# Performance work log

Hardware: AMD Instinct MI355X
Metric: run time of the kernel (lower is better)

## Reference

```python
import jax, jax.numpy as jnp
import numpy as np

N_NODES = 100000
N_GRAPHS = 64


def gcn_conv(x, src, dst, W, b, num_nodes):
    """PyG GCNConv: add self-loops, symmetric deg normalization, aggregate at dst."""
    h = x @ W  # [N, out]
    ones_e = jnp.ones(src.shape[0], dtype=x.dtype)
    # degree includes self-loop (+1)
    deg = jax.ops.segment_sum(ones_e, dst, num_segments=num_nodes) + 1.0
    dinv = jnp.where(deg > 0, 1.0 / jnp.sqrt(deg), 0.0)  # deg>=1 always here
    norm = dinv[src] * dinv[dst]  # [E]
    msg = h[src] * norm[:, None]  # gather + scale
    agg = jax.ops.segment_sum(msg, dst, num_segments=num_nodes)
    # self-loop contribution: norm_ii = dinv[i]^2
    agg = agg + h * (dinv * dinv)[:, None]
    return agg + b


def global_mean_pool(x, batch, num_graphs):
    sums = jax.ops.segment_sum(x, batch, num_segments=num_graphs)
    counts = jax.ops.segment_sum(jnp.ones(x.shape[0], dtype=x.dtype), batch,
                                 num_segments=num_graphs)
    return sums / jnp.maximum(counts, 1.0)[:, None]


def setup_inputs() -> dict:
    key = jax.random.key(0)
    ks = jax.random.split(key, 8)
    H = 128
    x = jax.random.normal(ks[0], (N_NODES, 4), dtype=jnp.float32)
    edge_index = jax.random.randint(ks[1], (2, 1600000), 0, N_NODES, dtype=jnp.int64 if jax.config.read('jax_enable_x64') else jnp.int32)
    batch = jnp.sort(jax.random.randint(ks[2], (N_NODES,), 0, N_GRAPHS))
    def glorot(k, shape):
        fan_in, fan_out = shape
        lim = np.sqrt(6.0 / (fan_in + fan_out))
        return jax.random.uniform(k, shape, jnp.float32, -lim, lim)
    return {
        'x': x,
        'edge_index': edge_index,
        'batch': batch,
        'W1': glorot(ks[3], (4, H)), 'b1': jnp.zeros((H,), jnp.float32),
        'W2': glorot(ks[4], (H, H)), 'b2': jnp.zeros((H,), jnp.float32),
        'W3': glorot(ks[5], (H, H)), 'b3': jnp.zeros((H,), jnp.float32),
        'Wl': glorot(ks[6], (H, 2)), 'bl': jnp.zeros((2,), jnp.float32),
    }


def reference(x, edge_index, batch, W1, b1, W2, b2, W3, b3, Wl, bl):
    src, dst = edge_index[0], edge_index[1]
    h = jax.nn.relu(gcn_conv(x, src, dst, W1, b1, N_NODES))
    h = jax.nn.relu(gcn_conv(h, src, dst, W2, b2, N_NODES))
    h = jax.nn.relu(gcn_conv(h, src, dst, W3, b3, N_NODES))
    g = global_mean_pool(h, batch, N_GRAPHS)  # [G, H]
    logits = g @ Wl + bl  # [G, 2]
    return jax.nn.log_softmax(logits, axis=1)
```

## Files before the change

### kernel.cpp

```cpp
#include <hip/hip_runtime.h>

#define HDIM 128
#define NGRAPH 64

#define BSHIFT 9
#define NBUCK 196
#define BCAP 48
#define BSTR 49
#define RCAP 9216
#define BIN_CHUNK 4096

typedef __attribute__((ext_vector_type(8))) short short8;
typedef __attribute__((ext_vector_type(4))) float floatx4;
typedef __attribute__((ext_vector_type(2))) float floatx2;

__device__ __forceinline__ float bf2f(unsigned short u) {
    union { unsigned int i; float f; } v;
    v.i = ((unsigned int)u) << 16;
    return v.f;
}
__device__ __forceinline__ unsigned short f2bf(float f) {
    unsigned int u = __float_as_uint(f);
    u += 0x7FFFu + ((u >> 16) & 1u);
    return (unsigned short)(u >> 16);
}

__global__ __launch_bounds__(256) void k_misc(int* __restrict__ gcur,
                                              const int* __restrict__ batch,
                                              float* __restrict__ gcnt,
                                              float* __restrict__ gsum,
                                              const float* __restrict__ W2,
                                              unsigned short* __restrict__ Wp2,
                                              const float* __restrict__ W3,
                                              unsigned short* __restrict__ Wp3,
                                              int N, int nbuck) {
    int t = threadIdx.x;
    int blk = blockIdx.x;
    if (blk == 0) {
        if (t < nbuck) gcur[t] = t * RCAP;
        for (int i = t; i < NGRAPH * 128; i += 256) gsum[i] = 0.f;
        if (t < NGRAPH) {
            int g = t;
            int lo = 0, hi = N;
            while (lo < hi) { int m = (lo + hi) >> 1; if (batch[m] < g) lo = m + 1; else hi = m; }
            int lb = lo;
            lo = 0; hi = N;
            while (lo < hi) { int m = (lo + hi) >> 1; if (batch[m] < g + 1) lo = m + 1; else hi = m; }
            gcnt[g] = (float)(lo - lb);
        }
        return;
    }
    const float* W = (blk <= 64) ? W2 : W3;
    unsigned short* Wp = (blk <= 64) ? Wp2 : Wp3;
    int idx = ((blk <= 64) ? (blk - 1) : (blk - 65)) * 256 + t;
    int j = idx & 7, l = (idx >> 3) & 63, frag = idx >> 9;
    int c = frag >> 2, ks = frag & 3;
    int k = ks * 32 + ((l >> 4) & 3) * 8 + j;
    int n = c * 16 + (l & 15);
    Wp[idx] = f2bf(W[k * 128 + n]);
}


__global__ __launch_bounds__(256) void k_binA(const int* __restrict__ src,
                                              const int* __restrict__ dst,
                                              int* __restrict__ gcur,
                                              unsigned int* __restrict__ binned, int E) {
    __shared__ unsigned int bin[NBUCK * BSTR];
    __shared__ int bcnt[NBUCK];
    __shared__ int bbase[NBUCK];
    int t = threadIdx.x;
    for (int b = t; b < NBUCK; b += 256) bcnt[b] = 0;
    __syncthreads();
    int e0 = blockIdx.x * BIN_CHUNK;
    #pragma unroll
    for (int i = 0; i < BIN_CHUNK / 1024; i++) {
        int e = e0 + i * 1024 + t * 4;
        if (e + 3 < E) {
            const int4 d4 = *(const int4*)&dst[e];
            const int4 s4 = *(const int4*)&src[e];
            int dd[4] = {d4.x, d4.y, d4.z, d4.w};
            int ss[4] = {s4.x, s4.y, s4.z, s4.w};
            #pragma unroll
            for (int k = 0; k < 4; k++) {
                int d = dd[k];
                unsigned int rec = ((unsigned int)(d & 511) << 20) | (unsigned int)ss[k];
                int b = d >> BSHIFT;
                int idx = atomicAdd(&bcnt[b], 1);
                if (idx < BCAP) bin[b * BSTR + idx] = rec;
                else { int p = atomicAdd(&gcur[b], 1); binned[p] = rec; }
            }
        } else {
            for (int k = 0; k < 4; k++) {
                int e2 = e + k;
                if (e2 < E) {
                    int d = dst[e2];
                    unsigned int rec = ((unsigned int)(d & 511) << 20) | (unsigned int)src[e2];
                    int b = d >> BSHIFT;
                    int idx = atomicAdd(&bcnt[b], 1);
                    if (idx < BCAP) bin[b * BSTR + idx] = rec;
                    else { int p = atomicAdd(&gcur[b], 1); binned[p] = rec; }
                }
            }
        }
    }
    __syncthreads();
    if (t < NBUCK) {
        int cnt = min(bcnt[t], BCAP);
        bbase[t] = atomicAdd(&gcur[t], cnt);
    }
    __syncthreads();
    int wave = t >> 6, lane = t & 63;
    for (int b = wave; b < NBUCK; b += 4) {
        int cnt = min(bcnt[b], BCAP);
        int base = bbase[b];
        if (lane < cnt) binned[base + lane] = bin[b * BSTR + lane];
    }
}

__global__ __launch_bounds__(256) void k_fillB(const int* __restrict__ gcur,
                                               const unsigned int* __restrict__ binned,
                                               int* __restrict__ P,
                                               float* __restrict__ dinv,
                                               int* __restrict__ csr,
                                               const float4* __restrict__ x4,
                                               float4* __restrict__ xs4,
                                               int N, int nbuck) {
    __shared__ int ps[256];
    __shared__ int cnt[512];
    __shared__ int image[RCAP];
    int b = blockIdx.x;
    int t = threadIdx.x;
    int lt = (t < nbuck) ? (gcur[t] - t * RCAP) : 0;
    ps[t] = lt;
    __syncthreads();
    for (int d = 1; d < 256; d <<= 1) {
        int o = (t >= d) ? ps[t - d] : 0;
        __syncthreads();
        ps[t] += o;
        __syncthreads();
    }
    int start = (b > 0) ? ps[b - 1] : 0;
    int len = ps[b] - start;
    __syncthreads();

    int n0 = b << BSHIFT;
    int nloc = min(n0 + 512, N) - n0;
    cnt[t] = 0; cnt[t + 256] = 0;
    __syncthreads();
    const unsigned int* rb = binned + (size_t)b * RCAP;
    for (int i = t; i < len; i += 256) atomicAdd(&cnt[rb[i] >> 20], 1);
    __syncthreads();
    int c0 = cnt[2 * t], c1 = cnt[2 * t + 1];
    int pair = c0 + c1;
    __syncthreads();
    cnt[t] = pair;
    __syncthreads();
    for (int d = 1; d < 256; d <<= 1) {
        int o = (t >= d) ? cnt[t - d] : 0;
        __syncthreads();
        cnt[t] += o;
        __syncthreads();
    }
    int excl = cnt[t] - pair;
    __syncthreads();
    if (2 * t < nloc) {
        int n = n0 + 2 * t;
        float dv0 = rsqrtf((float)c0 + 1.0f);
        P[n] = start + excl;
        dinv[n] = dv0;
        float4 xv = x4[n];
        xs4[n] = make_float4(xv.x * dv0, xv.y * dv0, xv.z * dv0, xv.w * dv0);
    }
    if (2 * t + 1 < nloc) {
        int n = n0 + 2 * t + 1;
        float dv1 = rsqrtf((float)c1 + 1.0f);
        P[n] = start + excl + c0;
        dinv[n] = dv1;
        float4 xv = x4[n];
        xs4[n] = make_float4(xv.x * dv1, xv.y * dv1, xv.z * dv1, xv.w * dv1);
    }
    if (b == nbuck - 1 && t == 0) P[N] = start + len;
    cnt[2 * t] = excl;
    cnt[2 * t + 1] = excl + c0;
    __syncthreads();
    for (int i = t; i < len; i += 256) {
        unsigned int rec = rb[i];
        int pos = atomicAdd(&cnt[rec >> 20], 1);
        image[pos] = (int)(rec & 0xFFFFFu);
    }
    __syncthreads();
    for (int i = t; i < len; i += 256) csr[start + i] = image[i];
}

__global__ void k_aggx_csr(const int* __restrict__ P, const int* __restrict__ csr,
                           const float4* __restrict__ xs, const float* __restrict__ dinv,
                           float4* __restrict__ aggx, int N) {
    int d = blockIdx.x * blockDim.x + threadIdx.x;
    if (d >= N) return;
    int s0 = P[d], s1 = P[d + 1];
    float dd = dinv[d];
    float4 sv = xs[d];
    float4 a = make_float4(sv.x * dd, sv.y * dd, sv.z * dd, sv.w * dd);
    int i = s0;
    int pre = min(s1, (s0 + 3) & ~3);
    for (; i < pre; i++) {
        float4 v = xs[csr[i]];
        a.x += v.x; a.y += v.y; a.z += v.z; a.w += v.w;
    }
    for (; i + 8 <= s1; i += 8) {
        const int4 iA = *(const int4*)&csr[i];
        const int4 iB = *(const int4*)&csr[i + 4];
        float4 vA = xs[iA.x], vB = xs[iA.y], vC = xs[iA.z], vD = xs[iA.w];
        float4 vE = xs[iB.x], vF = xs[iB.y], vG = xs[iB.z], vH = xs[iB.w];
        a.x += vA.x + vB.x + vC.x + vD.x + vE.x + vF.x + vG.x + vH.x;
        a.y += vA.y + vB.y + vC.y + vD.y + vE.y + vF.y + vG.y + vH.y;
        a.z += vA.z + vB.z + vC.z + vD.z + vE.z + vF.z + vG.z + vH.z;
        a.w += vA.w + vB.w + vC.w + vD.w + vE.w + vF.w + vG.w + vH.w;
    }
    for (; i + 4 <= s1; i += 4) {
        const int4 ix = *(const int4*)&csr[i];
        float4 vA = xs[ix.x], vB = xs[ix.y], vC = xs[ix.z], vD = xs[ix.w];
        a.x += vA.x + vB.x + vC.x + vD.x;
        a.y += vA.y + vB.y + vC.y + vD.y;
        a.z += vA.z + vB.z + vC.z + vD.z;
        a.w += vA.w + vB.w + vC.w + vD.w;
    }
    for (; i < s1; i++) {
        float4 v = xs[csr[i]];
        a.x += v.x; a.y += v.y; a.z += v.z; a.w += v.w;
    }
    aggx[d] = make_float4(a.x * dd, a.y * dd, a.z * dd, a.w * dd);
}

#define LXS 136
__global__ __launch_bounds__(256) void k_l1t2(const float4* __restrict__ aggx,
                                              const float* __restrict__ W1,
                                              const float* __restrict__ b1,
                                              const unsigned short* __restrict__ Wp,
                                              const float* __restrict__ dinv,
                                              unsigned char* __restrict__ out8, int N) {
    __shared__ unsigned short lx[64 * LXS];
    __shared__ unsigned short lw[16384];
    __shared__ float w1s[512];
    __shared__ float b1s[128];
    __shared__ float ax[64][4];
    int t = threadIdx.x;
    int n0 = blockIdx.x * 64;

    for (int i = t; i < 512; i += 256) w1s[i] = W1[i];
    if (t < 128) b1s[t] = b1[t];
    if (t < 64) {
        float4 v = (n0 + t < N) ? aggx[n0 + t] : make_float4(0.f, 0.f, 0.f, 0.f);
        ax[t][0] = v.x; ax[t][1] = v.y; ax[t][2] = v.z; ax[t][3] = v.w;
    }
    for (int ch = t; ch < 2048; ch += 256)
        *(uint4*)&lw[ch * 8] = *(const uint4*)&Wp[ch * 8];
    __syncthreads();

    for (int i = t; i < 8192; i += 256) {
        int n = i >> 7, j = i & 127;
        float v = b1s[j] + ax[n][0] * w1s[j] + ax[n][1] * w1s[128 + j]
                         + ax[n][2] * w1s[256 + j] + ax[n][3] * w1s[384 + j];
        lx[n * LXS + j] = f2bf(fmaxf(v, 0.f));
    }
    __syncthreads();

    int w = t >> 6, lane = t & 63;
    int m0 = w * 16;
    int col = lane & 15, quad = lane >> 4;

    short8 afrag[4];
    #pragma unroll
    for (int ks = 0; ks < 4; ks++)
        afrag[ks] = *(const short8*)&lx[(m0 + col) * LXS + ks * 32 + quad * 8];

    float dv[4];
    #pragma unroll
    for (int r = 0; r < 4; r++) {
        int gn = n0 + m0 + quad * 4 + r;
        dv[r] = (gn < N) ? dinv[gn] : 0.0f;
    }

    #pragma unroll
    for (int c = 0; c < 8; c++) {
        floatx4 acc = {0.f, 0.f, 0.f, 0.f};
        #pragma unroll
        for (int ks = 0; ks < 4; ks++) {
            const short8 bfrag = *(const short8*)&lw[((c * 4 + ks) * 64 + lane) * 8];
            acc = __builtin_amdgcn_mfma_f32_16x16x32_bf16(afrag[ks], bfrag, acc, 0, 0, 0);
        }
        #pragma unroll
        for (int r = 0; r < 4; r++) {
            int gn = n0 + m0 + quad * 4 + r;
            if (gn < N) {
                float v = acc[r] * dv[r];
                out8[(size_t)gn * 128 + c * 16 + col] =
                    (unsigned char)(__builtin_amdgcn_cvt_pk_fp8_f32(v, v, 0, false) & 0xFF);
            }
        }
    }
}

__global__ __launch_bounds__(256) void k_transform_mfma(const unsigned short* __restrict__ in,
                                                        const unsigned short* __restrict__ Wp,
                                                        const float* __restrict__ dinv,
                                                        unsigned char* __restrict__ out8, int N) {
    __shared__ unsigned short lx[64 * LXS];
    __shared__ unsigned short lw[16384];
    int t = threadIdx.x;
    int n0 = blockIdx.x * 64;

    for (int ch = t; ch < 1024; ch += 256) {
        int row = ch >> 4, part = ch & 15;
        uint4 val = make_uint4(0, 0, 0, 0);
        if (n0 + row < N) val = *(const uint4*)&in[(size_t)(n0 + row) * 128 + part * 8];
        *(uint4*)&lx[row * LXS + part * 8] = val;
    }
    for (int ch = t; ch < 2048; ch += 256)
        *(uint4*)&lw[ch * 8] = *(const uint4*)&Wp[ch * 8];
    __syncthreads();

    int w = t >> 6, lane = t & 63;
    int m0 = w * 16;
    int col = lane & 15, quad = lane >> 4;

    short8 afrag[4];
    #pragma unroll
    for (int ks = 0; ks < 4; ks++)
        afrag[ks] = *(const short8*)&lx[(m0 + col) * LXS + ks * 32 + quad * 8];

    float dv[4];
    #pragma unroll
    for (int r = 0; r < 4; r++) {
        int gn = n0 + m0 + quad * 4 + r;
        dv[r] = (gn < N) ? dinv[gn] : 0.0f;
    }

    #pragma unroll
    for (int c = 0; c < 8; c++) {
        floatx4 acc = {0.f, 0.f, 0.f, 0.f};
        #pragma unroll
        for (int ks = 0; ks < 4; ks++) {
            const short8 bfrag = *(const short8*)&lw[((c * 4 + ks) * 64 + lane) * 8];
            acc = __builtin_amdgcn_mfma_f32_16x16x32_bf16(afrag[ks], bfrag, acc, 0, 0, 0);
        }
        #pragma unroll
        for (int r = 0; r < 4; r++) {
            int gn = n0 + m0 + quad * 4 + r;
            if (gn < N) {
                float v = acc[r] * dv[r];
                out8[(size_t)gn * 128 + c * 16 + col] =
                    (unsigned char)(__builtin_amdgcn_cvt_pk_fp8_f32(v, v, 0, false) & 0xFF);
            }
        }
    }
}

__device__ __forceinline__ void fp8acc(unsigned int u, float& a0, float& a1,
                                       float& a2, float& a3) {
    floatx2 lo = __builtin_amdgcn_cvt_pk_f32_fp8(u, false);
    floatx2 hi = __builtin_amdgcn_cvt_pk_f32_fp8(u, true);
    a0 += lo.x; a1 += lo.y; a2 += hi.x; a3 += hi.y;
}

__device__ __forceinline__ void gather_fp8(const int* __restrict__ csr,
                                           const unsigned int* __restrict__ hs8,
                                           int s0, int s1, int lane,
                                           float& a0, float& a1, float& a2, float& a3) {
    int i = s0;
    int pre = min(s1, (s0 + 3) & ~3);
    for (; i < pre; i++)
        fp8acc(hs8[(size_t)csr[i] * 32 + lane], a0, a1, a2, a3);
    for (; i + 8 <= s1; i += 8) {
        const int4 iA = *(const int4*)&csr[i];
        const int4 iB = *(const int4*)&csr[i + 4];
        unsigned int u0 = hs8[(size_t)iA.x * 32 + lane];
        unsigned int u1 = hs8[(size_t)iA.y * 32 + lane];
        unsigned int u2 = hs8[(size_t)iA.z * 32 + lane];
        unsigned int u3 = hs8[(size_t)iA.w * 32 + lane];
        unsigned int u4 = hs8[(size_t)iB.x * 32 + lane];
        unsigned int u5 = hs8[(size_t)iB.y * 32 + lane];
        unsigned int u6 = hs8[(size_t)iB.z * 32 + lane];
        unsigned int u7 = hs8[(size_t)iB.w * 32 + lane];
        fp8acc(u0, a0, a1, a2, a3); fp8acc(u1, a0, a1, a2, a3);
        fp8acc(u2, a0, a1, a2, a3); fp8acc(u3, a0, a1, a2, a3);
        fp8acc(u4, a0, a1, a2, a3); fp8acc(u5, a0, a1, a2, a3);
        fp8acc(u6, a0, a1, a2, a3); fp8acc(u7, a0, a1, a2, a3);
    }
    for (; i + 4 <= s1; i += 4) {
        const int4 iA = *(const int4*)&csr[i];
        unsigned int u0 = hs8[(size_t)iA.x * 32 + lane];
        unsigned int u1 = hs8[(size_t)iA.y * 32 + lane];
        unsigned int u2 = hs8[(size_t)iA.z * 32 + lane];
        unsigned int u3 = hs8[(size_t)iA.w * 32 + lane];
        fp8acc(u0, a0, a1, a2, a3); fp8acc(u1, a0, a1, a2, a3);
        fp8acc(u2, a0, a1, a2, a3); fp8acc(u3, a0, a1, a2, a3);
    }
    for (; i < s1; i++)
        fp8acc(hs8[(size_t)csr[i] * 32 + lane], a0, a1, a2, a3);
}

__global__ __launch_bounds__(256) void k_agg_csr(const int* __restrict__ P,
                                                 const int* __restrict__ csr,
                                                 const unsigned int* __restrict__ hs8,
                                                 const float* __restrict__ dinv,
                                                 const float* __restrict__ bias,
                                                 unsigned short* __restrict__ out16,
                                                 const int* __restrict__ batch,
                                                 float* __restrict__ gsum,
                                                 int N, int mode) {
    __shared__ float psum[8][128];
    int t = threadIdx.x;
    int g = (blockIdx.x * 256 + t) >> 5;
    int lane = t & 31;
    int node = t >> 5;

    float o0 = 0.f, o1 = 0.f, o2 = 0.f, o3 = 0.f;
    if (g < N) {
        int s0 = P[g], s1 = P[g + 1];
        unsigned int su = hs8[(size_t)g * 32 + lane];
        floatx2 slo = __builtin_amdgcn_cvt_pk_f32_fp8(su, false);
        floatx2 shi = __builtin_amdgcn_cvt_pk_f32_fp8(su, true);
        float a0 = slo.x, a1 = slo.y, a2 = shi.x, a3 = shi.y;
        gather_fp8(csr, hs8, s0, s1, lane, a0, a1, a2, a3);
        float dd = dinv[g];
        const float4 bb = *(const float4*)&bias[lane * 4];
        o0 = fmaxf(a0 * dd + bb.x, 0.f);
        o1 = fmaxf(a1 * dd + bb.y, 0.f);
        o2 = fmaxf(a2 * dd + bb.z, 0.f);
        o3 = fmaxf(a3 * dd + bb.w, 0.f);
        if (mode == 0) {
            ushort4 o;
            o.x = f2bf(o0); o.y = f2bf(o1); o.z = f2bf(o2); o.w = f2bf(o3);
            *(ushort4*)&out16[(size_t)g * 128 + lane * 4] = o;
        }
    }
    if (mode != 0) {
        *(float4*)&psum[node][lane * 4] = make_float4(o0, o1, o2, o3);
        __syncthreads();
        if (t < 128) {
            int gb0 = blockIdx.x * 8;
            if (gb0 < N) {
                int glast = min(gb0 + 7, N - 1);
                int b0 = batch[gb0], bL = batch[glast];
                if (b0 == bL && gb0 + 7 < N) {
                    float s = psum[0][t] + psum[1][t] + psum[2][t] + psum[3][t]
                            + psum[4][t] + psum[5][t] + psum[6][t] + psum[7][t];
                    unsafeAtomicAdd(&gsum[(size_t)b0 * 128 + t], s);
                } else {
                    #pragma unroll
                    for (int r = 0; r < 8; r++)
                        if (gb0 + r < N)
                            unsafeAtomicAdd(&gsum[(size_t)batch[gb0 + r] * 128 + t],
                                            psum[r][t]);
                }
            }
        }
    }
}

__global__ __launch_bounds__(256) void k_head(const float* __restrict__ gsum,
                                              const float* __restrict__ gcnt,
                                              const float* __restrict__ Wl,
                                              const float* __restrict__ bl,
                                              float* __restrict__ out, int G) {
    int t = threadIdx.x;
    int g = t >> 2, q = t & 3;
    if (g >= G) return;
    float l0 = 0.f, l1 = 0.f;
    #pragma unroll
    for (int k = 0; k < 32; k++) {
        int jj = q * 32 + k;
        float v = gsum[(size_t)g * 128 + jj];
        l0 += v * Wl[jj * 2 + 0];
        l1 += v * Wl[jj * 2 + 1];
    }
    l0 += __shfl_xor(l0, 1, 64); l1 += __shfl_xor(l1, 1, 64);
    l0 += __shfl_xor(l0, 2, 64); l1 += __shfl_xor(l1, 2, 64);
    if (q == 0) {
        float inv = 1.0f / fmaxf(gcnt[g], 1.0f);
        l0 = l0 * inv + bl[0];
        l1 = l1 * inv + bl[1];
        float m = fmaxf(l0, l1);
        float lse = m + logf(expf(l0 - m) + expf(l1 - m));
        out[g * 2 + 0] = l0 - lse;
        out[g * 2 + 1] = l1 - lse;
    }
}


extern "C" void kernel_launch(void* const* d_in, const int* in_sizes, int n_in,
                              void* d_out, int out_size, void* d_ws, size_t ws_size,
                              hipStream_t stream) {
    const float* x   = (const float*)d_in[0];
    const int*   ei  = (const int*)d_in[1];
    const int*   bat = (const int*)d_in[2];
    const float* W1  = (const float*)d_in[3];
    const float* b1  = (const float*)d_in[4];
    const float* W2  = (const float*)d_in[5];
    const float* b2  = (const float*)d_in[6];
    const float* W3  = (const float*)d_in[7];
    const float* b3  = (const float*)d_in[8];
    const float* Wl  = (const float*)d_in[9];
    const float* bl  = (const float*)d_in[10];

    const int N = in_sizes[0] / 4;
    const int E = in_sizes[1] / 2;
    const int* srcI = ei;
    const int* dstI = ei + E;

    const int nbuck = (N + 511) >> BSHIFT;
    const int pAlloc = ((N + 1 + 3) & ~3) + 4;

    float* wsf  = (float*)d_ws;
    float* dinv = wsf;
    int*   P    = (int*)(dinv + N);
    int*   csr  = P + pAlloc;
    float* aggx = (float*)(csr + E);
    unsigned short* bufA16 = (unsigned short*)(aggx + (size_t)N * 4);
    unsigned char*  hs8    = (unsigned char*)(bufA16 + (size_t)N * 128);
    unsigned short* Wp2    = (unsigned short*)(hs8 + (size_t)N * 128);
    unsigned short* Wp3    = Wp2 + 16384;
    float* gsum = (float*)(Wp3 + 16384);
    float* gcnt = gsum + NGRAPH * 128;
    int*   gcur = (int*)(gcnt + NGRAPH);
    unsigned int* binned = (unsigned int*)hs8;
    float* xs4 = (float*)bufA16;

    k_misc<<<129, 256, 0, stream>>>(gcur, bat, gcnt, gsum, W2, Wp2, W3, Wp3, N, nbuck);
    k_binA<<<(E + BIN_CHUNK - 1) / BIN_CHUNK, 256, 0, stream>>>(srcI, dstI, gcur, binned, E);
    k_fillB<<<nbuck, 256, 0, stream>>>(gcur, binned, P, dinv, csr,
                                       (const float4*)x, (float4*)xs4, N, nbuck);

    k_aggx_csr<<<(N + 255) / 256, 256, 0, stream>>>(P, csr, (const float4*)xs4, dinv,
                                                    (float4*)aggx, N);
    k_l1t2<<<(N + 63) / 64, 256, 0, stream>>>((const float4*)aggx, W1, b1, Wp2, dinv, hs8, N);

    k_agg_csr<<<(N * 32 + 255) / 256, 256, 0, stream>>>(P, csr, (const unsigned int*)hs8,
                                                        dinv, b2, bufA16, nullptr, nullptr,
                                                        N, 0);

    k_transform_mfma<<<(N + 63) / 64, 256, 0, stream>>>(bufA16, Wp3, dinv, hs8, N);
    k_agg_csr<<<(N * 32 + 255) / 256, 256, 0, stream>>>(P, csr, (const unsigned int*)hs8,
                                                        dinv, b3, nullptr, bat, gsum, N, 1);

    k_head<<<1, 256, 0, stream>>>(gsum, gcnt, Wl, bl, (float*)d_out, NGRAPH);
}
```

Measured before the change: 314.7 us.

## Slice fp8 feature table into per-XCD column slabs for aggregation

The fp8 transformed features are now written in four 32-column slabs laid out node-major, so each slab is a contiguous table of 32 bytes per node. The aggregation kernel maps block IDs to XCDs so that each pair of XCDs gathers only one slab. Each XCD's L2 then caches a quarter of the feature table, which is meant to raise the gather hit rate. In exchange each node's CSR neighbour list is read four times, one 8-lane group handles one node-slice, and the mean-pool reduction now runs per slice with run-length batching.

```diff
diff --git a/kernel.cpp b/kernel.cpp
--- a/kernel.cpp
+++ b/kernel.cpp
@@ -289,12 +289,14 @@
             const short8 bfrag = *(const short8*)&lw[((c * 4 + ks) * 64 + lane) * 8];
             acc = __builtin_amdgcn_mfma_f32_16x16x32_bf16(afrag[ks], bfrag, acc, 0, 0, 0);
         }
+        int j = c * 16 + col;
+        size_t sbase = (size_t)(j >> 5) * N * 32 + (size_t)(j & 31);
         #pragma unroll
         for (int r = 0; r < 4; r++) {
             int gn = n0 + m0 + quad * 4 + r;
             if (gn < N) {
                 float v = acc[r] * dv[r];
-                out8[(size_t)gn * 128 + c * 16 + col] =
+                out8[sbase + (size_t)gn * 32] =
                     (unsigned char)(__builtin_amdgcn_cvt_pk_fp8_f32(v, v, 0, false) & 0xFF);
             }
         }
@@ -344,12 +346,14 @@
             const short8 bfrag = *(const short8*)&lw[((c * 4 + ks) * 64 + lane) * 8];
             acc = __builtin_amdgcn_mfma_f32_16x16x32_bf16(afrag[ks], bfrag, acc, 0, 0, 0);
         }
+        int j = c * 16 + col;
+        size_t sbase = (size_t)(j >> 5) * N * 32 + (size_t)(j & 31);
         #pragma unroll
         for (int r = 0; r < 4; r++) {
             int gn = n0 + m0 + quad * 4 + r;
             if (gn < N) {
                 float v = acc[r] * dv[r];
-                out8[(size_t)gn * 128 + c * 16 + col] =
+                out8[sbase + (size_t)gn * 32] =
                     (unsigned char)(__builtin_amdgcn_cvt_pk_fp8_f32(v, v, 0, false) & 0xFF);
             }
         }
@@ -363,25 +367,25 @@
     a0 += lo.x; a1 += lo.y; a2 += hi.x; a3 += hi.y;
 }
 
-__device__ __forceinline__ void gather_fp8(const int* __restrict__ csr,
-                                           const unsigned int* __restrict__ hs8,
-                                           int s0, int s1, int lane,
-                                           float& a0, float& a1, float& a2, float& a3) {
+__device__ __forceinline__ void gather8(const int* __restrict__ csr,
+                                        const unsigned int* __restrict__ stab,
+                                        int s0, int s1,
+                                        float& a0, float& a1, float& a2, float& a3) {
     int i = s0;
     int pre = min(s1, (s0 + 3) & ~3);
     for (; i < pre; i++)
-        fp8acc(hs8[(size_t)csr[i] * 32 + lane], a0, a1, a2, a3);
+        fp8acc(stab[(size_t)csr[i] * 8], a0, a1, a2, a3);
     for (; i + 8 <= s1; i += 8) {
         const int4 iA = *(const int4*)&csr[i];
         const int4 iB = *(const int4*)&csr[i + 4];
-        unsigned int u0 = hs8[(size_t)iA.x * 32 + lane];
-        unsigned int u1 = hs8[(size_t)iA.y * 32 + lane];
-        unsigned int u2 = hs8[(size_t)iA.z * 32 + lane];
-        unsigned int u3 = hs8[(size_t)iA.w * 32 + lane];
-        unsigned int u4 = hs8[(size_t)iB.x * 32 + lane];
-        unsigned int u5 = hs8[(size_t)iB.y * 32 + lane];
-        unsigned int u6 = hs8[(size_t)iB.z * 32 + lane];
-        unsigned int u7 = hs8[(size_t)iB.w * 32 + lane];
+        unsigned int u0 = stab[(size_t)iA.x * 8];
+        unsigned int u1 = stab[(size_t)iA.y * 8];
+        unsigned int u2 = stab[(size_t)iA.z * 8];
+        unsigned int u3 = stab[(size_t)iA.w * 8];
+        unsigned int u4 = stab[(size_t)iB.x * 8];
+        unsigned int u5 = stab[(size_t)iB.y * 8];
+        unsigned int u6 = stab[(size_t)iB.z * 8];
+        unsigned int u7 = stab[(size_t)iB.w * 8];
         fp8acc(u0, a0, a1, a2, a3); fp8acc(u1, a0, a1, a2, a3);
         fp8acc(u2, a0, a1, a2, a3); fp8acc(u3, a0, a1, a2, a3);
         fp8acc(u4, a0, a1, a2, a3); fp8acc(u5, a0, a1, a2, a3);
@@ -389,42 +393,48 @@
     }
     for (; i + 4 <= s1; i += 4) {
         const int4 iA = *(const int4*)&csr[i];
-        unsigned int u0 = hs8[(size_t)iA.x * 32 + lane];
-        unsigned int u1 = hs8[(size_t)iA.y * 32 + lane];
-        unsigned int u2 = hs8[(size_t)iA.z * 32 + lane];
-        unsigned int u3 = hs8[(size_t)iA.w * 32 + lane];
+        unsigned int u0 = stab[(size_t)iA.x * 8];
+        unsigned int u1 = stab[(size_t)iA.y * 8];
+        unsigned int u2 = stab[(size_t)iA.z * 8];
+        unsigned int u3 = stab[(size_t)iA.w * 8];
         fp8acc(u0, a0, a1, a2, a3); fp8acc(u1, a0, a1, a2, a3);
         fp8acc(u2, a0, a1, a2, a3); fp8acc(u3, a0, a1, a2, a3);
     }
     for (; i < s1; i++)
-        fp8acc(hs8[(size_t)csr[i] * 32 + lane], a0, a1, a2, a3);
-}
-
-__global__ __launch_bounds__(256) void k_agg_csr(const int* __restrict__ P,
-                                                 const int* __restrict__ csr,
-                                                 const unsigned int* __restrict__ hs8,
-                                                 const float* __restrict__ dinv,
-                                                 const float* __restrict__ bias,
-                                                 unsigned short* __restrict__ out16,
-                                                 const int* __restrict__ batch,
-                                                 float* __restrict__ gsum,
-                                                 int N, int mode) {
-    __shared__ float psum[8][128];
-    int t = threadIdx.x;
-    int g = (blockIdx.x * 256 + t) >> 5;
-    int lane = t & 31;
-    int node = t >> 5;
+        fp8acc(stab[(size_t)csr[i] * 8], a0, a1, a2, a3);
+}
+
+__global__ __launch_bounds__(256) void k_agg_sl(const int* __restrict__ P,
+                                                const int* __restrict__ csr,
+                                                const unsigned int* __restrict__ tab,
+                                                const float* __restrict__ dinv,
+                                                const float* __restrict__ bias,
+                                                unsigned short* __restrict__ out16,
+                                                const int* __restrict__ batch,
+                                                float* __restrict__ gsum,
+                                                int N, int mode) {
+    __shared__ float psum[32][32];
+    int t = threadIdx.x;
+    int bid = blockIdx.x;
+    int xcd = bid & 7;
+    int slice = xcd >> 1;
+    int chunk = (bid >> 3) * 2 + (xcd & 1);
+    int nb = chunk * 32;
+    int grp = t >> 3;
+    int l = t & 7;
+    int g = nb + grp;
+    const unsigned int* stab = tab + (size_t)slice * N * 8 + l;
 
     float o0 = 0.f, o1 = 0.f, o2 = 0.f, o3 = 0.f;
     if (g < N) {
         int s0 = P[g], s1 = P[g + 1];
-        unsigned int su = hs8[(size_t)g * 32 + lane];
+        unsigned int su = stab[(size_t)g * 8];
         floatx2 slo = __builtin_amdgcn_cvt_pk_f32_fp8(su, false);
         floatx2 shi = __builtin_amdgcn_cvt_pk_f32_fp8(su, true);
         float a0 = slo.x, a1 = slo.y, a2 = shi.x, a3 = shi.y;
-        gather_fp8(csr, hs8, s0, s1, lane, a0, a1, a2, a3);
+        gather8(csr, stab, s0, s1, a0, a1, a2, a3);
         float dd = dinv[g];
-        const float4 bb = *(const float4*)&bias[lane * 4];
+        const float4 bb = *(const float4*)&bias[slice * 32 + l * 4];
         o0 = fmaxf(a0 * dd + bb.x, 0.f);
         o1 = fmaxf(a1 * dd + bb.y, 0.f);
         o2 = fmaxf(a2 * dd + bb.z, 0.f);
@@ -432,28 +442,32 @@
         if (mode == 0) {
             ushort4 o;
             o.x = f2bf(o0); o.y = f2bf(o1); o.z = f2bf(o2); o.w = f2bf(o3);
-            *(ushort4*)&out16[(size_t)g * 128 + lane * 4] = o;
+            *(ushort4*)&out16[(size_t)g * 128 + slice * 32 + l * 4] = o;
         }
     }
     if (mode != 0) {
-        *(float4*)&psum[node][lane * 4] = make_float4(o0, o1, o2, o3);
+        *(float4*)&psum[grp][l * 4] = make_float4(o0, o1, o2, o3);
         __syncthreads();
-        if (t < 128) {
-            int gb0 = blockIdx.x * 8;
-            if (gb0 < N) {
-                int glast = min(gb0 + 7, N - 1);
-                int b0 = batch[gb0], bL = batch[glast];
-                if (b0 == bL && gb0 + 7 < N) {
-                    float s = psum[0][t] + psum[1][t] + psum[2][t] + psum[3][t]
-                            + psum[4][t] + psum[5][t] + psum[6][t] + psum[7][t];
-                    unsafeAtomicAdd(&gsum[(size_t)b0 * 128 + t], s);
-                } else {
-                    #pragma unroll
-                    for (int r = 0; r < 8; r++)
-                        if (gb0 + r < N)
-                            unsafeAtomicAdd(&gsum[(size_t)batch[gb0 + r] * 128 + t],
-                                            psum[r][t]);
+        if (t < 32 && nb < N) {
+            int f = t;
+            int nbN = min(32, N - nb);
+            int b0 = batch[nb], bL = batch[nb + nbN - 1];
+            if (b0 == bL) {
+                float s = 0.f;
+                #pragma unroll
+                for (int n = 0; n < 32; n++) s += psum[n][f];
+                unsafeAtomicAdd(&gsum[(size_t)b0 * 128 + slice * 32 + f], s);
+            } else {
+                float acc = 0.f; int cur = b0;
+                for (int n = 0; n < nbN; n++) {
+                    int bb = batch[nb + n];
+                    if (bb != cur) {
+                        unsafeAtomicAdd(&gsum[(size_t)cur * 128 + slice * 32 + f], acc);
+                        acc = 0.f; cur = bb;
+                    }
+                    acc += psum[n][f];
                 }
+                unsafeAtomicAdd(&gsum[(size_t)cur * 128 + slice * 32 + f], acc);
             }
         }
     }
@@ -527,6 +541,9 @@
     unsigned int* binned = (unsigned int*)hs8;
     float* xs4 = (float*)bufA16;
 
+    const int chunks = (N + 31) >> 5;
+    const int aggGrid = ((chunks + 1) >> 1) * 8;
+
     k_misc<<<129, 256, 0, stream>>>(gcur, bat, gcnt, gsum, W2, Wp2, W3, Wp3, N, nbuck);
     k_binA<<<(E + BIN_CHUNK - 1) / BIN_CHUNK, 256, 0, stream>>>(srcI, dstI, gcur, binned, E);
     k_fillB<<<nbuck, 256, 0, stream>>>(gcur, binned, P, dinv, csr,
@@ -536,13 +553,12 @@
                                                     (float4*)aggx, N);
     k_l1t2<<<(N + 63) / 64, 256, 0, stream>>>((const float4*)aggx, W1, b1, Wp2, dinv, hs8, N);
 
-    k_agg_csr<<<(N * 32 + 255) / 256, 256, 0, stream>>>(P, csr, (const unsigned int*)hs8,
-                                                        dinv, b2, bufA16, nullptr, nullptr,
-                                                        N, 0);
+    k_agg_sl<<<aggGrid, 256, 0, stream>>>(P, csr, (const unsigned int*)hs8,
+                                          dinv, b2, bufA16, nullptr, nullptr, N, 0);
 
     k_transform_mfma<<<(N + 63) / 64, 256, 0, stream>>>(bufA16, Wp3, dinv, hs8, N);
-    k_agg_csr<<<(N * 32 + 255) / 256, 256, 0, stream>>>(P, csr, (const unsigned int*)hs8,
-                                                        dinv, b3, nullptr, bat, gsum, N, 1);
+    k_agg_sl<<<aggGrid, 256, 0, stream>>>(P, csr, (const unsigned int*)hs8,
+                                          dinv, b3, nullptr, bat, gsum, N, 1);
 
     k_head<<<1, 256, 0, stream>>>(gsum, gcnt, Wl, bl, (float*)d_out, NGRAPH);
 }
```

New measurement: 305.1 us. -3.1%, faster.
